# Performance work log

Hardware: AMD Instinct MI355X
Metric: run time of the kernel (lower is better)

## Reference

```python
import jax, jax.numpy as jnp
import numpy as np

B, S, D = 1, 2048, 2048
H, KV = 32, 8
HD = D // H          # 64
R = H // KV          # 4 (GQA repeat factor)
ROPE_BASE = 10000.0


def setup_inputs() -> dict:
    key = jax.random.key(0)
    ks = jax.random.split(key, 5)
    x = jax.random.normal(ks[0], (B, S, D), jnp.float32)
    # Real rotary frequencies as (cos, sin) pairs: [S, HD//2, 2]
    inv_freq = 1.0 / (ROPE_BASE ** (np.arange(0, HD, 2, dtype=np.float64) / HD))
    ang = np.outer(np.arange(S, dtype=np.float64), inv_freq)
    freqs_cis = jnp.asarray(np.stack([np.cos(ang), np.sin(ang)], axis=-1), jnp.float32)
    std = 0.02
    wq = jax.random.normal(ks[1], (H * HD, D), jnp.float32) * std
    wk = jax.random.normal(ks[2], (KV * HD, D), jnp.float32) * std
    wv = jax.random.normal(ks[3], (KV * HD, D), jnp.float32) * std
    wo = jax.random.normal(ks[4], (D, H * HD), jnp.float32) * std
    return {"x": x, "freqs_cis": freqs_cis, "wq": wq, "wk": wk, "wv": wv, "wo": wo}


def _apply_rope(x, cos, sin):
    # x: [b, s, h, hd]; cos/sin: [s, hd//2]. Complex multiply on interleaved pairs.
    xr = x.reshape(*x.shape[:-1], HD // 2, 2)
    x0, x1 = xr[..., 0], xr[..., 1]
    c = cos[None, :, None, :]
    s = sin[None, :, None, :]
    o0 = x0 * c - x1 * s
    o1 = x0 * s + x1 * c
    return jnp.stack([o0, o1], axis=-1).reshape(x.shape)


def reference(x, freqs_cis, wq, wk, wv, wo):
    b, s, _ = x.shape
    q = (x @ wq.T).reshape(b, s, H, HD)
    k = (x @ wk.T).reshape(b, s, KV, HD)
    v = (x @ wv.T).reshape(b, s, KV, HD)
    cos, sin = freqs_cis[..., 0], freqs_cis[..., 1]
    q = _apply_rope(q, cos, sin)
    k = _apply_rope(k, cos, sin)
    # GQA: group q heads instead of repeat_interleave on k/v.
    # repeat_interleave maps kv-head g -> q heads [g*R, (g+1)*R), matching this reshape.
    qg = q.reshape(b, s, KV, R, HD)
    scale = 1.0 / np.sqrt(HD)
    scores = jnp.einsum('bsgrd,btgd->bgrst', qg, k) * scale  # [b, KV, R, s, t]
    causal = jnp.tril(jnp.ones((s, s), dtype=bool))
    scores = jnp.where(causal, scores, jnp.float32(-1e9))
    attn = jax.nn.softmax(scores.astype(jnp.float32), axis=-1).astype(q.dtype)
    out = jnp.einsum('bgrst,btgd->bsgrd', attn, v).reshape(b, s, H * HD)
    return out @ wo.T
```

## Files before the change

### kernel.cpp

```cpp
#include <hip/hip_runtime.h>

typedef unsigned short u16;
typedef unsigned int u32;
typedef __bf16 bf16x8 __attribute__((ext_vector_type(8)));
typedef unsigned short ushort8 __attribute__((ext_vector_type(8)));
typedef float floatx4 __attribute__((ext_vector_type(4)));
typedef u32 u32x2 __attribute__((ext_vector_type(2)));

#define S_LEN 2048
#define NH 32
#define NKV 8
#define HD_ 64
#define LDQ 3072

__device__ __forceinline__ u16 f2bf(float f) {
  unsigned u = __builtin_bit_cast(unsigned, f);
  u += 0x7FFF + ((u >> 16) & 1);
  return (u16)(u >> 16);
}
__device__ __forceinline__ float bf2f(u16 h) {
  unsigned u = ((unsigned)h) << 16;
  return __builtin_bit_cast(float, u);
}
__device__ __forceinline__ bf16x8 ld8(const u16* p) {
  return __builtin_bit_cast(bf16x8, *(const ushort8*)p);
}
__device__ __forceinline__ floatx4 mfma16(bf16x8 a, bf16x8 b, floatx4 c) {
  return __builtin_amdgcn_mfma_f32_16x16x32_bf16(a, b, c, 0, 0, 0);
}
__device__ __forceinline__ u32 pk2bf(float a, float b) {
  u32 ua = __builtin_bit_cast(u32, a) + 0x8000u;
  u32 ub = __builtin_bit_cast(u32, b) + 0x8000u;
  return __builtin_amdgcn_perm(ub, ua, 0x07060302);
}

__global__ void cvt_kernel(const float* __restrict__ in, u16* __restrict__ out, int n4) {
  int i = blockIdx.x * blockDim.x + threadIdx.x;
  if (i >= n4) return;
  float4 v = ((const float4*)in)[i];
  ((ushort4*)out)[i] = make_ushort4(f2bf(v.x), f2bf(v.y), f2bf(v.z), f2bf(v.w));
}

template <int TM, int TN, int OUT_BF16>
__global__ __launch_bounds__(256) void gemm_db(
    const u16* __restrict__ A, const u16* __restrict__ B, void* __restrict__ C,
    int ldc, int K, int lda) {
  __shared__ __align__(16) u16 As[2][TM * 64];
  __shared__ __align__(16) u16 Bs[2][TN * 64];
  const int tid = threadIdx.x;
  const int wave = tid >> 6, lane = tid & 63;
  const int quad = lane >> 4, l16 = lane & 15;
  const int bm = blockIdx.y * TM, bn = blockIdx.x * TN;
  const int wr = (wave >> 1) * (TM / 2), wc = (wave & 1) * (TN / 2);
  constexpr int MI = TM / 32, NI = TN / 32;
  const int crow = tid >> 3, col8 = tid & 7;

  size_t aoff[MI], boff[NI];
#pragma unroll
  for (int j = 0; j < MI; j++) aoff[j] = (size_t)(bm + crow + j * 32) * lda + col8 * 8;
#pragma unroll
  for (int j = 0; j < NI; j++) boff[j] = (size_t)(bn + crow + j * 32) * K + col8 * 8;

  ushort8 a8[MI], b8[NI];
  auto load_tiles = [&](int k0) {
#pragma unroll
    for (int j = 0; j < MI; j++) a8[j] = *(const ushort8*)(A + aoff[j] + k0);
#pragma unroll
    for (int j = 0; j < NI; j++) b8[j] = *(const ushort8*)(B + boff[j] + k0);
  };
  auto write_tiles = [&](int p) {
#pragma unroll
    for (int j = 0; j < MI; j++) {
      const int row = crow + j * 32;
      *(ushort8*)&As[p][row * 64 + ((col8 ^ (row & 7)) * 8)] = a8[j];
    }
#pragma unroll
    for (int j = 0; j < NI; j++) {
      const int row = crow + j * 32;
      *(ushort8*)&Bs[p][row * 64 + ((col8 ^ (row & 7)) * 8)] = b8[j];
    }
  };

  floatx4 acc[MI][NI] = {};
  load_tiles(0);
  write_tiles(0);
  __syncthreads();
  int p = 0;
  for (int k0 = 0; k0 < K; k0 += 64) {
    const bool more = (k0 + 64 < K);
    if (more) load_tiles(k0 + 64);
#pragma unroll
    for (int kh = 0; kh < 2; kh++) {
      bf16x8 af[MI], bfr[NI];
#pragma unroll
      for (int mi = 0; mi < MI; mi++) {
        const int row = wr + mi * 16 + l16;
        af[mi] = ld8(&As[p][row * 64 + (((kh * 4 + quad) ^ (row & 7)) * 8)]);
      }
#pragma unroll
      for (int ni = 0; ni < NI; ni++) {
        const int row = wc + ni * 16 + l16;
        bfr[ni] = ld8(&Bs[p][row * 64 + (((kh * 4 + quad) ^ (row & 7)) * 8)]);
      }
#pragma unroll
      for (int mi = 0; mi < MI; mi++)
#pragma unroll
        for (int ni = 0; ni < NI; ni++)
          acc[mi][ni] = mfma16(af[mi], bfr[ni], acc[mi][ni]);
    }
    if (more) {
      write_tiles(p ^ 1);
      __syncthreads();
      p ^= 1;
    }
  }

#pragma unroll
  for (int mi = 0; mi < MI; mi++)
#pragma unroll
    for (int ni = 0; ni < NI; ni++)
#pragma unroll
      for (int r = 0; r < 4; r++) {
        const int row = bm + wr + mi * 16 + quad * 4 + r;
        const int col = bn + wc + ni * 16 + l16;
        if (OUT_BF16) ((u16*)C)[(size_t)row * ldc + col] = f2bf(acc[mi][ni][r]);
        else          ((float*)C)[(size_t)row * ldc + col] = acc[mi][ni][r];
      }
}

__global__ void rope_kernel(u16* __restrict__ qk, const float* __restrict__ fc, int h_bits,
                            int row_stride, float scale) {
  int idx = blockIdx.x * blockDim.x + threadIdx.x;
  int d = idx & 31;
  int t = idx >> 5;
  int hh = t & ((1 << h_bits) - 1);
  int s = t >> h_bits;
  float c  = fc[s * 64 + d * 2];
  float sn = fc[s * 64 + d * 2 + 1];
  size_t base = (size_t)s * row_stride + hh * 64 + d * 2;
  float x0 = bf2f(qk[base]), x1 = bf2f(qk[base + 1]);
  qk[base]     = f2bf((x0 * c - x1 * sn) * scale);
  qk[base + 1] = f2bf((x0 * sn + x1 * c) * scale);
}

__global__ void transpose_v(const u16* __restrict__ qkv, u16* __restrict__ vT) {
  int idx = blockIdx.x * blockDim.x + threadIdx.x;
  int s = idx & (S_LEN - 1);
  int t = idx >> 11;
  vT[idx] = qkv[(size_t)s * LDQ + 2560 + t];
}

__global__ __launch_bounds__(256) void attn_kernel(const u16* qkv, const u16* __restrict__ vT,
                                                   u16* __restrict__ o) {
  __shared__ __align__(16) u16 Ks[2][64 * 64];
  __shared__ __align__(16) u16 Vs[2][64 * 64];
  __shared__ __align__(16) u16 pS[4][16 * 64];
  const int h = blockIdx.x;
  const int g = h >> 2;
  const int tid = threadIdx.x;
  const int wave = tid >> 6, lane = tid & 63;
  const int quad = lane >> 4, l16 = lane & 15;
  const int p_ = (int)blockIdx.y;
  const int qtB = 31 - p_;

  const ushort8 ones_u = {0x3F80, 0x3F80, 0x3F80, 0x3F80, 0x3F80, 0x3F80, 0x3F80, 0x3F80};
  const bf16x8 onesA = __builtin_bit_cast(bf16x8, ones_u);

  const int qrow = wave * 16 + l16;
  const int qgA = p_ * 64 + qrow, qgB = qtB * 64 + qrow;
  const size_t qoffA = (size_t)qgA * LDQ + h * HD_;
  const size_t qoffB = (size_t)qgB * LDQ + h * HD_;
  bf16x8 qfA0 = ld8(qkv + qoffA + quad * 8);
  bf16x8 qfA1 = ld8(qkv + qoffA + 32 + quad * 8);
  bf16x8 qfB0 = ld8(qkv + qoffB + quad * 8);
  bf16x8 qfB1 = ld8(qkv + qoffB + 32 + quad * 8);

  const int r0 = tid >> 3, r1 = r0 + 32;
  const int col8 = tid & 7;
  const int so = (col8 ^ (r0 & 7)) * 8;
  const int o0 = col8 * 8;
  const u16* ksrc = qkv + 2048 + g * HD_;
  const u16* vsrc = vT + (size_t)g * HD_ * S_LEN;

  ushort8 kp0, kp1, vp0, vp1;
  auto gload = [&](int t) {
    const int tb = t * 64;
    kp0 = *(const ushort8*)(ksrc + (size_t)(tb + r0) * LDQ + o0);
    kp1 = *(const ushort8*)(ksrc + (size_t)(tb + r1) * LDQ + o0);
    vp0 = *(const ushort8*)(vsrc + (size_t)r0 * S_LEN + tb + o0);
    vp1 = *(const ushort8*)(vsrc + (size_t)r1 * S_LEN + tb + o0);
  };
  auto tile_of = [&](int i) { return (i <= p_) ? i : (i - p_ - 1); };

  floatx4 OA[4] = {}, OB[4] = {};
  floatx4 lA = {}, lB = {};
  u16* myP = &pS[wave][0];

  gload(0);
  *(ushort8*)&Ks[0][r0 * 64 + so] = kp0;
  *(ushort8*)&Ks[0][r1 * 64 + so] = kp1;
  *(ushort8*)&Vs[0][r0 * 64 + so] = vp0;
  *(ushort8*)&Vs[0][r1 * 64 + so] = vp1;
  gload(tile_of(1));
  __syncthreads();
  int pp = 0;

  for (int i = 0; i < 33; i++) {
    const bool more = (i < 32);
    const bool isA = (i <= p_);
    const int kt = isA ? i : (i - p_ - 1);
    const int kbase = kt * 64;
    const int qg = isA ? qgA : qgB;
    const bf16x8 q0 = isA ? qfA0 : qfB0;
    const bf16x8 q1 = isA ? qfA1 : qfB1;

    const u16* Kc = &Ks[pp][0];
    const u16* Vc = &Vs[pp][0];
    bf16x8 kf[4][2], vf[4][2];
#pragma unroll
    for (int sub = 0; sub < 4; sub++) {
      const u16* kb = Kc + (sub * 16 + l16) * 64;
      kf[sub][0] = ld8(kb + ((quad ^ (l16 & 7)) * 8));
      kf[sub][1] = ld8(kb + (((4 + quad) ^ (l16 & 7)) * 8));
    }
#pragma unroll
    for (int nt = 0; nt < 4; nt++) {
      const u16* vb = Vc + (nt * 16 + l16) * 64;
      vf[nt][0] = ld8(vb + ((quad ^ (l16 & 7)) * 8));
      vf[nt][1] = ld8(vb + (((4 + quad) ^ (l16 & 7)) * 8));
    }

    if (more) {
      *(ushort8*)&Ks[pp ^ 1][r0 * 64 + so] = kp0;
      *(ushort8*)&Ks[pp ^ 1][r1 * 64 + so] = kp1;
      *(ushort8*)&Vs[pp ^ 1][r0 * 64 + so] = vp0;
      *(ushort8*)&Vs[pp ^ 1][r1 * 64 + so] = vp1;
      if (i < 31) gload(tile_of(i + 2));
    }

    floatx4 sf[4];
#pragma unroll
    for (int sub = 0; sub < 4; sub++) {
      floatx4 s = {};
      s = mfma16(kf[sub][0], q0, s);
      s = mfma16(kf[sub][1], q1, s);
      sf[sub] = s;
    }
    if (i == p_ || i == 32) {
#pragma unroll
      for (int sub = 0; sub < 4; sub++)
#pragma unroll
        for (int r = 0; r < 4; r++)
          if (kbase + sub * 16 + quad * 4 + r > qg) sf[sub][r] = -INFINITY;
    }

    u32x2 pk[4];
#pragma unroll
    for (int sub = 0; sub < 4; sub++) {
      pk[sub].x = pk2bf(__builtin_amdgcn_exp2f(sf[sub][0]), __builtin_amdgcn_exp2f(sf[sub][1]));
      pk[sub].y = pk2bf(__builtin_amdgcn_exp2f(sf[sub][2]), __builtin_amdgcn_exp2f(sf[sub][3]));
    }

#pragma unroll
    for (int sub = 0; sub < 4; sub++) {
      const int slot = (2 * sub + (quad >> 1)) ^ (l16 & 7);
      *(u32x2*)&myP[l16 * 64 + slot * 8 + (quad & 1) * 4] = pk[sub];
    }
    asm volatile("s_waitcnt lgkmcnt(0)" ::: "memory");
    bf16x8 pf0 = ld8(&myP[l16 * 64 + ((quad ^ (l16 & 7)) * 8)]);
    bf16x8 pf1 = ld8(&myP[l16 * 64 + (((4 + quad) ^ (l16 & 7)) * 8)]);

    if (isA) {
#pragma unroll
      for (int nt = 0; nt < 4; nt++) {
        OA[nt] = mfma16(vf[nt][0], pf0, OA[nt]);
        OA[nt] = mfma16(vf[nt][1], pf1, OA[nt]);
      }
      lA = mfma16(onesA, pf0, lA);
      lA = mfma16(onesA, pf1, lA);
    } else {
#pragma unroll
      for (int nt = 0; nt < 4; nt++) {
        OB[nt] = mfma16(vf[nt][0], pf0, OB[nt]);
        OB[nt] = mfma16(vf[nt][1], pf1, OB[nt]);
      }
      lB = mfma16(onesA, pf0, lB);
      lB = mfma16(onesA, pf1, lB);
    }

    if (more) {
      __syncthreads();
      pp ^= 1;
    }
  }

  const float invA = 1.0f / lA[0];
  const float invB = 1.0f / lB[0];
  const size_t ooffA = (size_t)qgA * 2048 + h * HD_;
  const size_t ooffB = (size_t)qgB * 2048 + h * HD_;
#pragma unroll
  for (int nt = 0; nt < 4; nt++)
#pragma unroll
    for (int r = 0; r < 4; r++) {
      const int hd = nt * 16 + quad * 4 + r;
      o[ooffA + hd] = f2bf(OA[nt][r] * invA);
      o[ooffB + hd] = f2bf(OB[nt][r] * invB);
    }
}

extern "C" void kernel_launch(void* const* d_in, const int* in_sizes, int n_in,
                              void* d_out, int out_size, void* d_ws, size_t ws_size,
                              hipStream_t stream) {
  const float* x  = (const float*)d_in[0];
  const float* fc = (const float*)d_in[1];
  const float* wq = (const float*)d_in[2];
  const float* wk = (const float*)d_in[3];
  const float* wv = (const float*)d_in[4];
  const float* wo = (const float*)d_in[5];
  float* out = (float*)d_out;

  char* ws = (char*)d_ws;
  const size_t MB = 1024 * 1024;
  u16* qkv = (u16*)(ws);
  u16* wb  = (u16*)(ws + 12 * MB);
  u16* vTb = (u16*)(ws + 12 * MB);
  u16* wob = (u16*)(ws + 14 * MB);
  u16* ob  = (u16*)(ws + 22 * MB);
  u16* xb  = (u16*)d_out;
  (void)ws_size; (void)n_in; (void)in_sizes; (void)out_size;

  cvt_kernel<<<4096, 256, 0, stream>>>(x,  xb, 1048576);
  cvt_kernel<<<4096, 256, 0, stream>>>(wq, wb, 1048576);
  cvt_kernel<<<1024, 256, 0, stream>>>(wk, wb + (size_t)2048 * 2048, 262144);
  cvt_kernel<<<1024, 256, 0, stream>>>(wv, wb + (size_t)2560 * 2048, 262144);
  gemm_db<128, 64, 1><<<dim3(48, 16), 256, 0, stream>>>(xb, wb, qkv, LDQ, 2048, 2048);
  cvt_kernel<<<4096, 256, 0, stream>>>(wo, wob, 1048576);
  rope_kernel<<<8192, 256, 0, stream>>>(qkv, fc, 5, LDQ, 0.18033688f);
  rope_kernel<<<2048, 256, 0, stream>>>(qkv + 2048, fc, 3, LDQ, 1.0f);
  transpose_v<<<4096, 256, 0, stream>>>(qkv, vTb);
  attn_kernel<<<dim3(NH, 16), 256, 0, stream>>>(qkv, vTb, ob);
  gemm_db<64, 64, 0><<<dim3(32, 32), 256, 0, stream>>>(ob, wob, out, 2048, 2048, 2048);
}
```

Measured before the change: 245.3 us.

## Split attention loop into per-query-tile phases and retile both GEMMs

The single 33-iteration attention loop, which selected between the A and B query tiles on every step, is replaced by two sequential phases, each with its own accumulator set. This removes the per-iteration select and should reduce register pressure. V fragment loads move after the exponentials, and the block barrier becomes a raw s_barrier preceded by an explicit lgkmcnt wait. Separately, the QKV GEMM tile changes from 128x64 to 128x96 and the output GEMM from 64x64 to 128x64, which gives fewer, larger blocks and may lower occupancy or leave tail imbalance.

```diff
diff --git a/kernel.cpp b/kernel.cpp
--- a/kernel.cpp
+++ b/kernel.cpp
@@ -175,137 +175,119 @@
   bf16x8 qfB0 = ld8(qkv + qoffB + quad * 8);
   bf16x8 qfB1 = ld8(qkv + qoffB + 32 + quad * 8);
 
-  const int r0 = tid >> 3, r1 = r0 + 32;
+  const int rs0 = tid >> 3, rs1 = rs0 + 32;
   const int col8 = tid & 7;
-  const int so = (col8 ^ (r0 & 7)) * 8;
+  const int so = (col8 ^ (rs0 & 7)) * 8;
   const int o0 = col8 * 8;
+  const int x0 = (quad ^ (l16 & 7)) * 8;
+  const int x1 = ((4 + quad) ^ (l16 & 7)) * 8;
   const u16* ksrc = qkv + 2048 + g * HD_;
   const u16* vsrc = vT + (size_t)g * HD_ * S_LEN;
 
   ushort8 kp0, kp1, vp0, vp1;
   auto gload = [&](int t) {
     const int tb = t * 64;
-    kp0 = *(const ushort8*)(ksrc + (size_t)(tb + r0) * LDQ + o0);
-    kp1 = *(const ushort8*)(ksrc + (size_t)(tb + r1) * LDQ + o0);
-    vp0 = *(const ushort8*)(vsrc + (size_t)r0 * S_LEN + tb + o0);
-    vp1 = *(const ushort8*)(vsrc + (size_t)r1 * S_LEN + tb + o0);
+    kp0 = *(const ushort8*)(ksrc + (size_t)(tb + rs0) * LDQ + o0);
+    kp1 = *(const ushort8*)(ksrc + (size_t)(tb + rs1) * LDQ + o0);
+    vp0 = *(const ushort8*)(vsrc + (size_t)rs0 * S_LEN + tb + o0);
+    vp1 = *(const ushort8*)(vsrc + (size_t)rs1 * S_LEN + tb + o0);
   };
   auto tile_of = [&](int i) { return (i <= p_) ? i : (i - p_ - 1); };
 
-  floatx4 OA[4] = {}, OB[4] = {};
-  floatx4 lA = {}, lB = {};
   u16* myP = &pS[wave][0];
+  int pp = 0;
 
   gload(0);
-  *(ushort8*)&Ks[0][r0 * 64 + so] = kp0;
-  *(ushort8*)&Ks[0][r1 * 64 + so] = kp1;
-  *(ushort8*)&Vs[0][r0 * 64 + so] = vp0;
-  *(ushort8*)&Vs[0][r1 * 64 + so] = vp1;
+  *(ushort8*)&Ks[0][rs0 * 64 + so] = kp0;
+  *(ushort8*)&Ks[0][rs1 * 64 + so] = kp1;
+  *(ushort8*)&Vs[0][rs0 * 64 + so] = vp0;
+  *(ushort8*)&Vs[0][rs1 * 64 + so] = vp1;
   gload(tile_of(1));
   __syncthreads();
-  int pp = 0;
-
-  for (int i = 0; i < 33; i++) {
-    const bool more = (i < 32);
-    const bool isA = (i <= p_);
-    const int kt = isA ? i : (i - p_ - 1);
-    const int kbase = kt * 64;
-    const int qg = isA ? qgA : qgB;
-    const bf16x8 q0 = isA ? qfA0 : qfB0;
-    const bf16x8 q1 = isA ? qfA1 : qfB1;
-
-    const u16* Kc = &Ks[pp][0];
-    const u16* Vc = &Vs[pp][0];
-    bf16x8 kf[4][2], vf[4][2];
-#pragma unroll
-    for (int sub = 0; sub < 4; sub++) {
-      const u16* kb = Kc + (sub * 16 + l16) * 64;
-      kf[sub][0] = ld8(kb + ((quad ^ (l16 & 7)) * 8));
-      kf[sub][1] = ld8(kb + (((4 + quad) ^ (l16 & 7)) * 8));
-    }
-#pragma unroll
-    for (int nt = 0; nt < 4; nt++) {
-      const u16* vb = Vc + (nt * 16 + l16) * 64;
-      vf[nt][0] = ld8(vb + ((quad ^ (l16 & 7)) * 8));
-      vf[nt][1] = ld8(vb + (((4 + quad) ^ (l16 & 7)) * 8));
-    }
-
-    if (more) {
-      *(ushort8*)&Ks[pp ^ 1][r0 * 64 + so] = kp0;
-      *(ushort8*)&Ks[pp ^ 1][r1 * 64 + so] = kp1;
-      *(ushort8*)&Vs[pp ^ 1][r0 * 64 + so] = vp0;
-      *(ushort8*)&Vs[pp ^ 1][r1 * 64 + so] = vp1;
-      if (i < 31) gload(tile_of(i + 2));
-    }
-
-    floatx4 sf[4];
-#pragma unroll
-    for (int sub = 0; sub < 4; sub++) {
-      floatx4 s = {};
-      s = mfma16(kf[sub][0], q0, s);
-      s = mfma16(kf[sub][1], q1, s);
-      sf[sub] = s;
-    }
-    if (i == p_ || i == 32) {
-#pragma unroll
-      for (int sub = 0; sub < 4; sub++)
-#pragma unroll
-        for (int r = 0; r < 4; r++)
-          if (kbase + sub * 16 + quad * 4 + r > qg) sf[sub][r] = -INFINITY;
-    }
-
-    u32x2 pk[4];
-#pragma unroll
-    for (int sub = 0; sub < 4; sub++) {
-      pk[sub].x = pk2bf(__builtin_amdgcn_exp2f(sf[sub][0]), __builtin_amdgcn_exp2f(sf[sub][1]));
-      pk[sub].y = pk2bf(__builtin_amdgcn_exp2f(sf[sub][2]), __builtin_amdgcn_exp2f(sf[sub][3]));
-    }
-
-#pragma unroll
-    for (int sub = 0; sub < 4; sub++) {
-      const int slot = (2 * sub + (quad >> 1)) ^ (l16 & 7);
-      *(u32x2*)&myP[l16 * 64 + slot * 8 + (quad & 1) * 4] = pk[sub];
-    }
-    asm volatile("s_waitcnt lgkmcnt(0)" ::: "memory");
-    bf16x8 pf0 = ld8(&myP[l16 * 64 + ((quad ^ (l16 & 7)) * 8)]);
-    bf16x8 pf1 = ld8(&myP[l16 * 64 + (((4 + quad) ^ (l16 & 7)) * 8)]);
-
-    if (isA) {
+
+  auto phase = [&](int qt, int qg, bf16x8 q0, bf16x8 q1, int ibase) {
+    floatx4 O[4] = {};
+    floatx4 lac = {};
+    for (int kt = 0; kt <= qt; kt++) {
+      const int i = ibase + kt;
+      const u16* Kc = &Ks[pp][0];
+      const u16* Vc = &Vs[pp][0];
+
+      bf16x8 kf[4][2];
+#pragma unroll
+      for (int sub = 0; sub < 4; sub++) {
+        const u16* kb = Kc + (sub * 16 + l16) * 64;
+        kf[sub][0] = ld8(kb + x0);
+        kf[sub][1] = ld8(kb + x1);
+      }
+      if (i < 32) {
+        *(ushort8*)&Ks[pp ^ 1][rs0 * 64 + so] = kp0;
+        *(ushort8*)&Ks[pp ^ 1][rs1 * 64 + so] = kp1;
+        *(ushort8*)&Vs[pp ^ 1][rs0 * 64 + so] = vp0;
+        *(ushort8*)&Vs[pp ^ 1][rs1 * 64 + so] = vp1;
+        if (i < 31) gload(tile_of(i + 2));
+      }
+      floatx4 sf[4];
+#pragma unroll
+      for (int sub = 0; sub < 4; sub++) {
+        floatx4 s = {};
+        s = mfma16(kf[sub][0], q0, s);
+        s = mfma16(kf[sub][1], q1, s);
+        sf[sub] = s;
+      }
+      if (kt == qt) {
+#pragma unroll
+        for (int sub = 0; sub < 4; sub++)
+#pragma unroll
+          for (int r = 0; r < 4; r++)
+            if (kt * 64 + sub * 16 + quad * 4 + r > qg) sf[sub][r] = -INFINITY;
+      }
+      u32x2 pk[4];
+#pragma unroll
+      for (int sub = 0; sub < 4; sub++) {
+        pk[sub].x = pk2bf(__builtin_amdgcn_exp2f(sf[sub][0]), __builtin_amdgcn_exp2f(sf[sub][1]));
+        pk[sub].y = pk2bf(__builtin_amdgcn_exp2f(sf[sub][2]), __builtin_amdgcn_exp2f(sf[sub][3]));
+      }
+      bf16x8 vf[4][2];
 #pragma unroll
       for (int nt = 0; nt < 4; nt++) {
-        OA[nt] = mfma16(vf[nt][0], pf0, OA[nt]);
-        OA[nt] = mfma16(vf[nt][1], pf1, OA[nt]);
-      }
-      lA = mfma16(onesA, pf0, lA);
-      lA = mfma16(onesA, pf1, lA);
-    } else {
+        const u16* vb = Vc + (nt * 16 + l16) * 64;
+        vf[nt][0] = ld8(vb + x0);
+        vf[nt][1] = ld8(vb + x1);
+      }
+#pragma unroll
+      for (int sub = 0; sub < 4; sub++) {
+        const int slot = (2 * sub + (quad >> 1)) ^ (l16 & 7);
+        *(u32x2*)&myP[l16 * 64 + slot * 8 + (quad & 1) * 4] = pk[sub];
+      }
+      asm volatile("s_waitcnt lgkmcnt(0)" ::: "memory");
+      bf16x8 pf0 = ld8(&myP[l16 * 64 + x0]);
+      bf16x8 pf1 = ld8(&myP[l16 * 64 + x1]);
 #pragma unroll
       for (int nt = 0; nt < 4; nt++) {
-        OB[nt] = mfma16(vf[nt][0], pf0, OB[nt]);
-        OB[nt] = mfma16(vf[nt][1], pf1, OB[nt]);
-      }
-      lB = mfma16(onesA, pf0, lB);
-      lB = mfma16(onesA, pf1, lB);
-    }
-
-    if (more) {
-      __syncthreads();
-      pp ^= 1;
-    }
-  }
-
-  const float invA = 1.0f / lA[0];
-  const float invB = 1.0f / lB[0];
-  const size_t ooffA = (size_t)qgA * 2048 + h * HD_;
-  const size_t ooffB = (size_t)qgB * 2048 + h * HD_;
-#pragma unroll
-  for (int nt = 0; nt < 4; nt++)
-#pragma unroll
-    for (int r = 0; r < 4; r++) {
-      const int hd = nt * 16 + quad * 4 + r;
-      o[ooffA + hd] = f2bf(OA[nt][r] * invA);
-      o[ooffB + hd] = f2bf(OB[nt][r] * invB);
-    }
+        O[nt] = mfma16(vf[nt][0], pf0, O[nt]);
+        O[nt] = mfma16(vf[nt][1], pf1, O[nt]);
+      }
+      lac = mfma16(onesA, pf0, lac);
+      lac = mfma16(onesA, pf1, lac);
+
+      if (i < 32) {
+        asm volatile("s_waitcnt lgkmcnt(0)" ::: "memory");
+        __builtin_amdgcn_s_barrier();
+        pp ^= 1;
+      }
+    }
+    const float inv = 1.0f / lac[0];
+    const size_t ooff = (size_t)qg * 2048 + h * HD_;
+#pragma unroll
+    for (int nt = 0; nt < 4; nt++)
+#pragma unroll
+      for (int r = 0; r < 4; r++)
+        o[ooff + nt * 16 + quad * 4 + r] = f2bf(O[nt][r] * inv);
+  };
+
+  phase(p_, qgA, qfA0, qfA1, 0);
+  phase(qtB, qgB, qfB0, qfB1, p_ + 1);
 }
 
 extern "C" void kernel_launch(void* const* d_in, const int* in_sizes, int n_in,
@@ -333,11 +315,11 @@
   cvt_kernel<<<4096, 256, 0, stream>>>(wq, wb, 1048576);
   cvt_kernel<<<1024, 256, 0, stream>>>(wk, wb + (size_t)2048 * 2048, 262144);
   cvt_kernel<<<1024, 256, 0, stream>>>(wv, wb + (size_t)2560 * 2048, 262144);
-  gemm_db<128, 64, 1><<<dim3(48, 16), 256, 0, stream>>>(xb, wb, qkv, LDQ, 2048, 2048);
+  gemm_db<128, 96, 1><<<dim3(32, 16), 256, 0, stream>>>(xb, wb, qkv, LDQ, 2048, 2048);
   cvt_kernel<<<4096, 256, 0, stream>>>(wo, wob, 1048576);
   rope_kernel<<<8192, 256, 0, stream>>>(qkv, fc, 5, LDQ, 0.18033688f);
   rope_kernel<<<2048, 256, 0, stream>>>(qkv + 2048, fc, 3, LDQ, 1.0f);
   transpose_v<<<4096, 256, 0, stream>>>(qkv, vTb);
   attn_kernel<<<dim3(NH, 16), 256, 0, stream>>>(qkv, vTb, ob);
-  gemm_db<64, 64, 0><<<dim3(32, 32), 256, 0, stream>>>(ob, wob, out, 2048, 2048, 2048);
-}
+  gemm_db<128, 64, 0><<<dim3(32, 16), 256, 0, stream>>>(ob, wob, out, 2048, 2048, 2048);
+}
```

Result: faster. 227.3 us (-7.3%).
